# Optimization experiments

Measured on AMD Instinct MI355X. Metric: run time of the kernel, lower is better.

## Reference

```python
import jax, jax.numpy as jnp
import numpy as np

K = 32        # num_classes
NQ = 16384    # num query samples
C = 512       # feature_dim
H_REF = 512   # refinement_net hidden
H_CONF = 256  # confidence_net hidden
NUM_STEPS = 3


def setup_inputs() -> dict:
    key = jax.random.key(0)
    ks = jax.random.split(key, 8)
    s = 0.02
    return {
        "prototypes": jax.random.normal(ks[0], (K, C), jnp.float32),
        "query_features": jax.random.normal(ks[1], (NQ, C), jnp.float32),
        "query_distances": jax.random.uniform(ks[2], (NQ, K), jnp.float32) * 10.0,
        "W1": jax.random.normal(ks[3], (2 * C, H_REF), jnp.float32) * s,
        "b1": jnp.zeros((H_REF,), jnp.float32),
        "W2": jax.random.normal(ks[4], (H_REF, C), jnp.float32) * s,
        "b2": jnp.zeros((C,), jnp.float32),
        "Wc1": jax.random.normal(ks[5], (2 * C, H_CONF), jnp.float32) * s,
        "bc1": jnp.zeros((H_CONF,), jnp.float32),
        "Wc2": jax.random.normal(ks[6], (H_CONF, 1), jnp.float32) * s,
        "bc2": jnp.zeros((1,), jnp.float32),
    }


def reference(prototypes, query_features, query_distances,
              W1, b1, W2, b2, Wc1, bc1, Wc2, bc2):
    # ---- refinement loop (3 steps, sequential in refined prototypes) ----
    refined = prototypes
    for step in range(NUM_STEPS):
        # soft assignments over classes; temperature = step + 1
        soft = jax.nn.softmax(-query_distances / (step + 1.0), axis=-1)  # (NQ, K)
        wsum = jnp.maximum(soft.sum(axis=0), 1e-6)                       # (K,)  clamp(min=1e-6)
        wmean = (soft.T @ query_features) / wsum[:, None]                # (K, C)
        concat = jnp.concatenate([refined, wmean], axis=-1)              # (K, 2C)
        h = jax.nn.relu(concat @ W1 + b1)                                # dropout is identity in eval
        refinement = h @ W2 + b2                                         # (K, C)
        refined = refined + 0.1 * refinement

    # ---- confidence scores: MLP on [proto, query] pairs, mean over queries ----
    # Split first-layer weight into proto half and query half to avoid
    # materializing the (K, NQ, 2C) concat explicitly (same math).
    Wp, Wq = Wc1[:C], Wc1[C:]
    hp = prototypes @ Wp          # (K, H_CONF)
    hq = query_features @ Wq      # (NQ, H_CONF)
    hidden = jax.nn.relu(hp[:, None, :] + hq[None, :, :] + bc1)  # (K, NQ, H_CONF)
    conf = jax.nn.sigmoid(hidden @ Wc2 + bc2)                    # (K, NQ, 1)
    confidence_scores = conf.reshape(K, -1).mean(axis=1)         # (K,)

    return refined, confidence_scores
```

## Files before the change

### kernel.cpp

```cpp
#include <hip/hip_runtime.h>

#define KP 32
#define NQg 16384
#define CD 512
#define HC 256
#define NS 3

typedef __attribute__((ext_vector_type(8))) short short8;
typedef __attribute__((ext_vector_type(4))) short short4_t;
typedef __attribute__((ext_vector_type(8))) __bf16 bf16x8;
typedef __attribute__((ext_vector_type(4))) float floatx4;

union S8B8 { short8 s; bf16x8 b; };

__device__ __forceinline__ short f2bf(float f) {
    union { float f; unsigned u; } v; v.f = f;
    unsigned r = v.u + 0x7fffu + ((v.u >> 16) & 1u);
    return (short)(r >> 16);
}
__device__ __forceinline__ float bf2f(short s) {
    union { unsigned u; float f; } v; v.u = ((unsigned)(unsigned short)s) << 16;
    return v.f;
}
__device__ __forceinline__ float bflo(unsigned u) { return __uint_as_float(u << 16); }
__device__ __forceinline__ float bfhi(unsigned u) { return __uint_as_float(u & 0xffff0000u); }

__global__ __launch_bounds__(256) void k_A(const float* __restrict__ qd,
                                           const float* __restrict__ W1, const float* __restrict__ W2,
                                           const float* __restrict__ Wc1, const float* __restrict__ proto,
                                           const float* __restrict__ qf, const float* __restrict__ bc1,
                                           short* __restrict__ softT,
                                           short* __restrict__ W1p, short* __restrict__ W2p,
                                           short* __restrict__ wqp, float* __restrict__ refined,
                                           short* __restrict__ refined_b,
                                           short* __restrict__ qf2b, float* __restrict__ wmean,
                                           float* __restrict__ hpb,
                                           int* __restrict__ bar, float* __restrict__ dout) {
    int tid = threadIdx.x;
    int bid = blockIdx.x;
    if (bid < 64) {
        int q = bid * 256 + tid;
        float d[32];
        const float4* p = (const float4*)(qd + (size_t)q * 32);
#pragma unroll
        for (int j = 0; j < 8; j++) {
            float4 v = p[j];
            d[4 * j] = v.x; d[4 * j + 1] = v.y; d[4 * j + 2] = v.z; d[4 * j + 3] = v.w;
        }
#pragma unroll
        for (int s = 0; s < 3; s++) {
            float inv = -1.0f / (float)(s + 1);
            float e[32];
            float sum = 0.f;
#pragma unroll
            for (int k = 0; k < 32; k++) { e[k] = __expf(d[k] * inv); sum += e[k]; }
            float r = 1.0f / sum;
#pragma unroll
            for (int k = 0; k < 32; k++)
                softT[(size_t)(s * 32 + k) * NQg + q] = f2bf(e[k] * r);
        }
        return;
    }
    if (bid < 3712) {
        if (bid == 64) {
            if (tid < 32) dout[16384 + tid] = 0.f;
            else if (tid < 40) bar[tid - 32] = 0;
        }
        int idx = (bid - 64) * 256 + tid;
        if (idx < 524288) {
            int k = idx >> 9, n = idx & 511;
            W1p[((size_t)(k >> 3) * 512 + n) * 8 + (k & 7)] = f2bf(W1[idx]);
        } else if (idx < 786432) {
            int j = idx - 524288;
            int k = j >> 9, n = j & 511;
            W2p[((size_t)(k >> 3) * 512 + n) * 8 + (k & 7)] = f2bf(W2[j]);
        } else if (idx < 917504) {
            int j = idx - 786432;
            int k = j >> 8, n = j & 255;
            wqp[((size_t)(k >> 3) * 256 + n) * 8 + (k & 7)] = f2bf(Wc1[(size_t)(512 + k) * 256 + n]);
        } else {
            int j = idx - 917504;
            float v = proto[j];
            refined[j] = v;
            refined_b[j] = f2bf(v);
        }
        return;
    }
    if (bid < 3904) {
        int idx = (bid - 3712) * 256 + tid;
        wmean[idx] = 0.f;
        return;
    }
    if (bid < 5952) {
#pragma unroll
        for (int it = 0; it < 4; it++) {
            int j = (bid - 3904) * 1024 + it * 256 + tid;
            float4 v = *(const float4*)&qf[(size_t)j * 4];
            short4_t o;
            o[0] = f2bf(v.x); o[1] = f2bf(v.y); o[2] = f2bf(v.z); o[3] = f2bf(v.w);
            *(short4_t*)&qf2b[(size_t)j * 4] = o;
        }
        return;
    }
    {
        int r = bid - 5952;
        const float* pr = proto + r * 512;
        const float* wc = Wc1 + tid;
        float a0 = 0.f, a1 = 0.f, a2 = 0.f, a3 = 0.f;
#pragma unroll 4
        for (int i = 0; i < 512; i += 4) {
            float4 p4 = *(const float4*)&pr[i];
            float w0 = wc[(size_t)i * 256];
            float w1 = wc[(size_t)(i + 1) * 256];
            float w2 = wc[(size_t)(i + 2) * 256];
            float w3 = wc[(size_t)(i + 3) * 256];
            a0 += p4.x * w0;
            a1 += p4.y * w1;
            a2 += p4.z * w2;
            a3 += p4.w * w3;
        }
        hpb[r * 256 + tid] = bc1[tid] + ((a0 + a1) + (a2 + a3));
    }
}

__global__ __launch_bounds__(256) void k_B(const short* __restrict__ qf2b,
                                           const short* __restrict__ softT,
                                           const short* __restrict__ wqp,
                                           float* __restrict__ wmean,
                                           short* __restrict__ hq_g,
                                           float* __restrict__ wsuminv) {
    __shared__ short B_lds[128 * 40];
    int tid = threadIdx.x;
    int lane = tid & 63, w = tid >> 6;
    int ml = lane & 15, q8 = lane >> 4;

    if (blockIdx.x < 256) {
        int kc = blockIdx.x >> 2, ns = blockIdx.x & 3;
        int c0 = ns * 128;
        int qbase0 = kc * 256;
        int c_l = 2 * lane;
        int q_l = 8 * w;

        floatx4 acc[6][2];
#pragma unroll
        for (int mt = 0; mt < 6; mt++)
#pragma unroll
            for (int nt = 0; nt < 2; nt++) acc[mt][nt] = (floatx4){0.f, 0.f, 0.f, 0.f};

        for (int step = 0; step < 8; step++) {
            int qb = qbase0 + step * 32;
            short8 sA, sB;
#pragma unroll
            for (int i = 0; i < 8; i++) {
                unsigned u = *(const unsigned*)&qf2b[(size_t)(qb + q_l + i) * 512 + c0 + c_l];
                sA[i] = (short)(u & 0xffffu);
                sB[i] = (short)(u >> 16);
            }
            __syncthreads();
            *(short8*)&B_lds[c_l * 40 + q_l] = sA;
            *(short8*)&B_lds[(c_l + 1) * 40 + q_l] = sB;
            S8B8 a[6];
#pragma unroll
            for (int mt = 0; mt < 6; mt++)
                a[mt].s = *(const short8*)&softT[(size_t)(mt * 16 + ml) * NQg + qb + q8 * 8];
            __syncthreads();
#pragma unroll
            for (int nt = 0; nt < 2; nt++) {
                S8B8 b; b.s = *(short8*)&B_lds[(w * 32 + nt * 16 + ml) * 40 + q8 * 8];
#pragma unroll
                for (int mt = 0; mt < 6; mt++)
                    acc[mt][nt] = __builtin_amdgcn_mfma_f32_16x16x32_bf16(a[mt].b, b.b, acc[mt][nt], 0, 0, 0);
            }
        }
#pragma unroll
        for (int mt = 0; mt < 6; mt++) {
#pragma unroll
            for (int nt = 0; nt < 2; nt++) {
                int c = c0 + w * 32 + nt * 16 + ml;
#pragma unroll
                for (int r = 0; r < 4; r++) {
                    int m = mt * 16 + q8 * 4 + r;
                    atomicAdd(&wmean[(size_t)m * 512 + c], acc[mt][nt][r]);
                }
            }
        }
    } else if (blockIdx.x < 768) {
        int m0 = (blockIdx.x - 256) * 32;
        int n0 = w * 64;
        floatx4 acc[2][4];
#pragma unroll
        for (int mt = 0; mt < 2; mt++)
#pragma unroll
            for (int nt = 0; nt < 4; nt++) acc[mt][nt] = (floatx4){0.f, 0.f, 0.f, 0.f};

#pragma unroll 4
        for (int kc = 0; kc < 512; kc += 32) {
            S8B8 a[2], b[4];
#pragma unroll
            for (int mt = 0; mt < 2; mt++)
                a[mt].s = *(const short8*)&qf2b[(size_t)(m0 + mt * 16 + ml) * 512 + kc + q8 * 8];
#pragma unroll
            for (int nt = 0; nt < 4; nt++)
                b[nt].s = *(const short8*)&wqp[((size_t)((kc >> 3) + q8) * 256 + n0 + nt * 16 + ml) * 8];
#pragma unroll
            for (int mt = 0; mt < 2; mt++)
#pragma unroll
                for (int nt = 0; nt < 4; nt++)
                    acc[mt][nt] = __builtin_amdgcn_mfma_f32_16x16x32_bf16(a[mt].b, b[nt].b, acc[mt][nt], 0, 0, 0);
        }
#pragma unroll
        for (int mt = 0; mt < 2; mt++)
#pragma unroll
            for (int nt = 0; nt < 4; nt++) {
                int col = n0 + nt * 16 + ml;
#pragma unroll
                for (int r = 0; r < 4; r++) {
                    int row = m0 + mt * 16 + q8 * 4 + r;
                    hq_g[(size_t)row * 256 + col] = f2bf(acc[mt][nt][r]);
                }
            }
    } else {
        float* red = (float*)B_lds;
        int sk = blockIdx.x - 768;
        const short* row = softT + (size_t)sk * NQg;
        float s = 0.f;
#pragma unroll
        for (int j = 0; j < 8; j++) {
            short8 v = *(const short8*)&row[j * 2048 + tid * 8];
#pragma unroll
            for (int i = 0; i < 8; i++) s += bf2f(v[i]);
        }
        red[tid] = s;
        __syncthreads();
        for (int off = 128; off > 0; off >>= 1) {
            if (tid < off) red[tid] += red[tid + off];
            __syncthreads();
        }
        if (tid == 0) wsuminv[sk] = 1.0f / fmaxf(red[0], 1e-6f);
    }
}

__device__ __forceinline__ void gbar(int* bar, int phase, int nblk) {
    __syncthreads();
    if (threadIdx.x == 0) {
        __threadfence();
        __hip_atomic_fetch_add(&bar[phase], 1, __ATOMIC_ACQ_REL, __HIP_MEMORY_SCOPE_AGENT);
        while (__hip_atomic_load(&bar[phase], __ATOMIC_ACQUIRE, __HIP_MEMORY_SCOPE_AGENT) < nblk)
            __builtin_amdgcn_s_sleep(1);
    }
    __syncthreads();
}

__global__ __launch_bounds__(256) void k_D(const float* __restrict__ wmean,
                                           const float* __restrict__ wsuminv,
                                           const short* __restrict__ W1p,
                                           const float* __restrict__ b1,
                                           const short* __restrict__ W2p,
                                           const float* __restrict__ b2,
                                           float* __restrict__ refined,
                                           short* __restrict__ hb,
                                           int* __restrict__ bar,
                                           const short* __restrict__ hq_g,
                                           const float* __restrict__ hpb,
                                           const float* __restrict__ Wc2,
                                           const float* __restrict__ bc2p,
                                           float* __restrict__ dout,
                                           short* __restrict__ wmean_b,
                                           short* __restrict__ refined_b) {
    __shared__ float smem[6688];
    int tid = threadIdx.x, lane = tid & 63, w = tid >> 6;
    int ml = lane & 15, q8 = lane >> 4;

    if (blockIdx.x < 16) {
        int nb = blockIdx.x;
        int nh = w & 1, mh = w >> 1;
        int n = nb * 32 + nh * 16 + ml;
        int phase = 0;

#pragma unroll
        for (int i = 0; i < 12; i++) {
            int idx = i * 4096 + nb * 256 + tid;
            int row = idx >> 9;
            wmean_b[idx] = f2bf(wmean[idx] * wsuminv[row]);
        }
        gbar(bar, phase++, 16);

        for (int s = 0; s < 3; s++) {
            {
                const short* rfb = refined_b + (size_t)(mh * 16 + ml) * 512;
                const short* wmb = wmean_b + (size_t)(s * 32 + mh * 16 + ml) * 512;
                floatx4 acc = (floatx4){0.f, 0.f, 0.f, 0.f};
#pragma unroll
                for (int st = 0; st < 16; st++) {
                    int k0 = st * 32 + q8 * 8;
                    S8B8 a; a.s = *(const short8*)&rfb[k0];
                    S8B8 b; b.s = *(const short8*)&W1p[((size_t)(k0 >> 3) * 512 + n) * 8];
                    acc = __builtin_amdgcn_mfma_f32_16x16x32_bf16(a.b, b.b, acc, 0, 0, 0);
                }
#pragma unroll
                for (int st = 16; st < 32; st++) {
                    int k0 = st * 32 + q8 * 8;
                    S8B8 a; a.s = *(const short8*)&wmb[k0 - 512];
                    S8B8 b; b.s = *(const short8*)&W1p[((size_t)(k0 >> 3) * 512 + n) * 8];
                    acc = __builtin_amdgcn_mfma_f32_16x16x32_bf16(a.b, b.b, acc, 0, 0, 0);
                }
                float bias = b1[n];
#pragma unroll
                for (int r = 0; r < 4; r++) {
                    int row = mh * 16 + q8 * 4 + r;
                    hb[(size_t)row * 512 + n] = f2bf(fmaxf(acc[r] + bias, 0.f));
                }
            }
            gbar(bar, phase++, 16);
            {
                floatx4 acc = (floatx4){0.f, 0.f, 0.f, 0.f};
#pragma unroll
                for (int st = 0; st < 16; st++) {
                    int k0 = st * 32 + q8 * 8;
                    S8B8 a; a.s = *(const short8*)&hb[(size_t)(mh * 16 + ml) * 512 + k0];
                    S8B8 b; b.s = *(const short8*)&W2p[((size_t)(k0 >> 3) * 512 + n) * 8];
                    acc = __builtin_amdgcn_mfma_f32_16x16x32_bf16(a.b, b.b, acc, 0, 0, 0);
                }
                float b2v = b2[n];
#pragma unroll
                for (int r = 0; r < 4; r++) {
                    int row = mh * 16 + q8 * 4 + r;
                    float val = refined[(size_t)row * 512 + n] + 0.1f * (acc[r] + b2v);
                    refined[(size_t)row * 512 + n] = val;
                    refined_b[(size_t)row * 512 + n] = f2bf(val);
                    if (s == 2) dout[(size_t)row * 512 + n] = val;
                }
            }
            if (s < 2) gbar(bar, phase++, 16);
        }
    } else {
        short* hq_lds = (short*)smem;
        short* hp_s   = (short*)smem + 4480;
        float* wc2s   = smem + 6400;
        float* confl  = smem + 6656;
        int q0 = (blockIdx.x - 16) * 16;

        wc2s[tid] = Wc2[tid];
        if (tid < 32) confl[tid] = 0.f;
#pragma unroll
        for (int i = 0; i < 8; i++) {
            int idx = i * 256 + tid;
            int r = idx >> 6, c = (idx & 63) * 4;
            float4 v = *(const float4*)&hpb[r * 256 + c];
            short4_t o;
            o[0] = f2bf(v.x); o[1] = f2bf(v.y); o[2] = f2bf(v.z); o[3] = f2bf(v.w);
            *(short4_t*)&hp_s[r * 260 + c] = o;
        }
        {
            const short* hqs = hq_g + (size_t)q0 * 256;
            int r = tid >> 4, c = (tid & 15) * 16;
            *(short8*)&hq_lds[r * 280 + c] = *(const short8*)&hqs[r * 256 + c];
            *(short8*)&hq_lds[r * 280 + c + 8] = *(const short8*)&hqs[r * 256 + c + 8];
        }
        __syncthreads();

        int q = tid & 15, kg = tid >> 4;
        int k0 = kg, k1 = kg + 16;
        float s0 = 0.f, s1 = 0.f;
        for (int h = 0; h < 256; h += 4) {
            uint2 hv = *(uint2*)&hq_lds[q * 280 + h];
            float f0 = bflo(hv.x), f1 = bfhi(hv.x), f2 = bflo(hv.y), f3 = bfhi(hv.y);
            uint2 u0 = *(uint2*)&hp_s[k0 * 260 + h];
            uint2 u1 = *(uint2*)&hp_s[k1 * 260 + h];
            float4 wv = *(float4*)&wc2s[h];
            s0 += fmaxf(bflo(u0.x) + f0, 0.f) * wv.x;
            s0 += fmaxf(bfhi(u0.x) + f1, 0.f) * wv.y;
            s0 += fmaxf(bflo(u0.y) + f2, 0.f) * wv.z;
            s0 += fmaxf(bfhi(u0.y) + f3, 0.f) * wv.w;
            s1 += fmaxf(bflo(u1.x) + f0, 0.f) * wv.x;
            s1 += fmaxf(bfhi(u1.x) + f1, 0.f) * wv.y;
            s1 += fmaxf(bflo(u1.y) + f2, 0.f) * wv.z;
            s1 += fmaxf(bfhi(u1.y) + f3, 0.f) * wv.w;
        }
        float bc2 = bc2p[0];
        float v0 = 1.f / (1.f + __expf(-(s0 + bc2)));
        float v1 = 1.f / (1.f + __expf(-(s1 + bc2)));
        atomicAdd(&confl[k0], v0);
        atomicAdd(&confl[k1], v1);
        __syncthreads();
        if (tid < 32) atomicAdd(&dout[16384 + tid], confl[tid] * (1.0f / 16384.0f));
    }
}

extern "C" void kernel_launch(void* const* d_in, const int* in_sizes, int n_in,
                              void* d_out, int out_size, void* d_ws, size_t ws_size,
                              hipStream_t stream) {
    const float* proto = (const float*)d_in[0];
    const float* qf    = (const float*)d_in[1];
    const float* qd    = (const float*)d_in[2];
    const float* W1    = (const float*)d_in[3];
    const float* b1    = (const float*)d_in[4];
    const float* W2    = (const float*)d_in[5];
    const float* b2    = (const float*)d_in[6];
    const float* Wc1   = (const float*)d_in[7];
    const float* bc1   = (const float*)d_in[8];
    const float* Wc2   = (const float*)d_in[9];
    const float* bc2   = (const float*)d_in[10];
    float* out = (float*)d_out;

    float* ws = (float*)d_ws;
    short* softT   = (short*)ws;
    short* qf2b    = (short*)(ws + 786432);
    float* wmean   = ws + 4980736;
    float* refined = ws + 5029888;
    short* hb      = (short*)(ws + 5046272);
    short* W1p     = (short*)(ws + 5054464);
    short* W2p     = (short*)(ws + 5316608);
    short* wqp     = (short*)(ws + 5447680);
    float* hpb     = ws + 5513216;
    int*   bar     = (int*)(ws + 5521408);
    float* wsuminv = ws + 5521416;
    short* hq      = (short*)(ws + 5521536);
    short* refined_b = (short*)(ws + 7618688);
    short* wmean_b   = (short*)(ws + 7626880);

    k_A<<<5984, 256, 0, stream>>>(qd, W1, W2, Wc1, proto, qf, bc1, softT, W1p, W2p, wqp,
                                  refined, refined_b, qf2b, wmean, hpb, bar, out);
    k_B<<<864, 256, 0, stream>>>(qf2b, softT, wqp, wmean, hq, wsuminv);
    k_D<<<1040, 256, 0, stream>>>(wmean, wsuminv, W1p, b1, W2p, b2, refined, hb, bar,
                                  hq, hpb, Wc2, bc2, out, wmean_b, refined_b);
}
```

Before: 194.1 us.

## Restructure refinement loop to split-K atomic accumulation, cutting grid barriers

The 16-block refinement path no longer keeps refined/refined_b and hb buffers in global memory. Each block computes its 32-column slice of h, keeps it in LDS, and atomically accumulates partial W2 products into per-step accumulators. The refined input is rebuilt on the fly from proto plus the earlier accumulators, and wmean normalization is fused into the A-operand load. This cuts the grid barriers per run from six to three, in exchange for float atomics, extra zeroing in k_A, and a different bf16 rounding path.

```diff
diff --git a/kernel.cpp b/kernel.cpp
--- a/kernel.cpp
+++ b/kernel.cpp
@@ -31,9 +31,9 @@
                                            const float* __restrict__ qf, const float* __restrict__ bc1,
                                            short* __restrict__ softT,
                                            short* __restrict__ W1p, short* __restrict__ W2p,
-                                           short* __restrict__ wqp, float* __restrict__ refined,
-                                           short* __restrict__ refined_b,
+                                           short* __restrict__ wqp,
                                            short* __restrict__ qf2b, float* __restrict__ wmean,
+                                           float* __restrict__ accs,
                                            float* __restrict__ hpb,
                                            int* __restrict__ bar, float* __restrict__ dout) {
     int tid = threadIdx.x;
@@ -61,11 +61,7 @@
         }
         return;
     }
-    if (bid < 3712) {
-        if (bid == 64) {
-            if (tid < 32) dout[16384 + tid] = 0.f;
-            else if (tid < 40) bar[tid - 32] = 0;
-        }
+    if (bid < 3648) {
         int idx = (bid - 64) * 256 + tid;
         if (idx < 524288) {
             int k = idx >> 9, n = idx & 511;
@@ -74,27 +70,27 @@
             int j = idx - 524288;
             int k = j >> 9, n = j & 511;
             W2p[((size_t)(k >> 3) * 512 + n) * 8 + (k & 7)] = f2bf(W2[j]);
-        } else if (idx < 917504) {
+        } else {
             int j = idx - 786432;
             int k = j >> 8, n = j & 255;
             wqp[((size_t)(k >> 3) * 256 + n) * 8 + (k & 7)] = f2bf(Wc1[(size_t)(512 + k) * 256 + n]);
-        } else {
-            int j = idx - 917504;
-            float v = proto[j];
-            refined[j] = v;
-            refined_b[j] = f2bf(v);
         }
         return;
     }
-    if (bid < 3904) {
-        int idx = (bid - 3712) * 256 + tid;
-        wmean[idx] = 0.f;
+    if (bid < 4032) {
+        if (bid == 3648) {
+            if (tid < 32) dout[16384 + tid] = 0.f;
+            else if (tid < 40) bar[tid - 32] = 0;
+        }
+        int idx = (bid - 3648) * 256 + tid;
+        if (idx < 49152) wmean[idx] = 0.f;
+        else accs[idx - 49152] = 0.f;
         return;
     }
-    if (bid < 5952) {
+    if (bid < 6080) {
 #pragma unroll
         for (int it = 0; it < 4; it++) {
-            int j = (bid - 3904) * 1024 + it * 256 + tid;
+            int j = (bid - 4032) * 1024 + it * 256 + tid;
             float4 v = *(const float4*)&qf[(size_t)j * 4];
             short4_t o;
             o[0] = f2bf(v.x); o[1] = f2bf(v.y); o[2] = f2bf(v.z); o[3] = f2bf(v.w);
@@ -103,7 +99,7 @@
         return;
     }
     {
-        int r = bid - 5952;
+        int r = bid - 6080;
         const float* pr = proto + r * 512;
         const float* wc = Wc1 + tid;
         float a0 = 0.f, a1 = 0.f, a2 = 0.f, a3 = 0.f;
@@ -257,81 +253,116 @@
                                            const float* __restrict__ b1,
                                            const short* __restrict__ W2p,
                                            const float* __restrict__ b2,
-                                           float* __restrict__ refined,
-                                           short* __restrict__ hb,
+                                           const float* __restrict__ proto,
+                                           float* __restrict__ accs,
                                            int* __restrict__ bar,
                                            const short* __restrict__ hq_g,
                                            const float* __restrict__ hpb,
                                            const float* __restrict__ Wc2,
                                            const float* __restrict__ bc2p,
-                                           float* __restrict__ dout,
-                                           short* __restrict__ wmean_b,
-                                           short* __restrict__ refined_b) {
+                                           float* __restrict__ dout) {
     __shared__ float smem[6688];
     int tid = threadIdx.x, lane = tid & 63, w = tid >> 6;
     int ml = lane & 15, q8 = lane >> 4;
 
     if (blockIdx.x < 16) {
+        short* hb_s = (short*)smem;
+        float* acc0 = accs;
+        float* acc1 = accs + 16384;
+        float* acc2 = accs + 32768;
         int nb = blockIdx.x;
-        int nh = w & 1, mh = w >> 1;
-        int n = nb * 32 + nh * 16 + ml;
-        int phase = 0;
-
-#pragma unroll
-        for (int i = 0; i < 12; i++) {
-            int idx = i * 4096 + nb * 256 + tid;
-            int row = idx >> 9;
-            wmean_b[idx] = f2bf(wmean[idx] * wsuminv[row]);
-        }
-        gbar(bar, phase++, 16);
-
+        int mh = w >> 1, nh = w & 1;
+        int n_loc = nh * 16 + ml;
+        int n = nb * 32 + n_loc;
+        float b1v = b1[n];
+        int arow = mh * 16 + ml;
+
+        const float* pr  = proto + (size_t)arow * 512;
+        const float* a0p = acc0 + (size_t)arow * 512;
+        const float* a1p = acc1 + (size_t)arow * 512;
+
+#pragma unroll
         for (int s = 0; s < 3; s++) {
-            {
-                const short* rfb = refined_b + (size_t)(mh * 16 + ml) * 512;
-                const short* wmb = wmean_b + (size_t)(s * 32 + mh * 16 + ml) * 512;
-                floatx4 acc = (floatx4){0.f, 0.f, 0.f, 0.f};
-#pragma unroll
-                for (int st = 0; st < 16; st++) {
-                    int k0 = st * 32 + q8 * 8;
-                    S8B8 a; a.s = *(const short8*)&rfb[k0];
-                    S8B8 b; b.s = *(const short8*)&W1p[((size_t)(k0 >> 3) * 512 + n) * 8];
-                    acc = __builtin_amdgcn_mfma_f32_16x16x32_bf16(a.b, b.b, acc, 0, 0, 0);
+            float iv = wsuminv[s * 32 + arow];
+            const float* wm = wmean + (size_t)(s * 32 + arow) * 512;
+            float sb2 = 0.1f * (float)s;
+            floatx4 ac[4];
+#pragma unroll
+            for (int j = 0; j < 4; j++) ac[j] = (floatx4){0.f, 0.f, 0.f, 0.f};
+
+#pragma unroll
+            for (int st = 0; st < 16; st++) {
+                int k0 = st * 32 + q8 * 8;
+                float f[8];
+                float4 pa = *(const float4*)&pr[k0];
+                float4 pb = *(const float4*)&pr[k0 + 4];
+                f[0] = pa.x; f[1] = pa.y; f[2] = pa.z; f[3] = pa.w;
+                f[4] = pb.x; f[5] = pb.y; f[6] = pb.z; f[7] = pb.w;
+                if (s >= 1) {
+                    float4 qa = *(const float4*)&a0p[k0];
+                    float4 qb = *(const float4*)&a0p[k0 + 4];
+                    f[0] += 0.1f * qa.x; f[1] += 0.1f * qa.y; f[2] += 0.1f * qa.z; f[3] += 0.1f * qa.w;
+                    f[4] += 0.1f * qb.x; f[5] += 0.1f * qb.y; f[6] += 0.1f * qb.z; f[7] += 0.1f * qb.w;
+                    float4 ba = *(const float4*)&b2[k0];
+                    float4 bb = *(const float4*)&b2[k0 + 4];
+                    f[0] += sb2 * ba.x; f[1] += sb2 * ba.y; f[2] += sb2 * ba.z; f[3] += sb2 * ba.w;
+                    f[4] += sb2 * bb.x; f[5] += sb2 * bb.y; f[6] += sb2 * bb.z; f[7] += sb2 * bb.w;
                 }
-#pragma unroll
-                for (int st = 16; st < 32; st++) {
-                    int k0 = st * 32 + q8 * 8;
-                    S8B8 a; a.s = *(const short8*)&wmb[k0 - 512];
-                    S8B8 b; b.s = *(const short8*)&W1p[((size_t)(k0 >> 3) * 512 + n) * 8];
-                    acc = __builtin_amdgcn_mfma_f32_16x16x32_bf16(a.b, b.b, acc, 0, 0, 0);
+                if (s >= 2) {
+                    float4 qa = *(const float4*)&a1p[k0];
+                    float4 qb = *(const float4*)&a1p[k0 + 4];
+                    f[0] += 0.1f * qa.x; f[1] += 0.1f * qa.y; f[2] += 0.1f * qa.z; f[3] += 0.1f * qa.w;
+                    f[4] += 0.1f * qb.x; f[5] += 0.1f * qb.y; f[6] += 0.1f * qb.z; f[7] += 0.1f * qb.w;
                 }
-                float bias = b1[n];
+                short8 t;
+#pragma unroll
+                for (int i = 0; i < 8; i++) t[i] = f2bf(f[i]);
+                S8B8 a; a.s = t;
+                S8B8 b; b.s = *(const short8*)&W1p[((size_t)(k0 >> 3) * 512 + n) * 8];
+                ac[st & 3] = __builtin_amdgcn_mfma_f32_16x16x32_bf16(a.b, b.b, ac[st & 3], 0, 0, 0);
+            }
+#pragma unroll
+            for (int st = 16; st < 32; st++) {
+                int kw = (st - 16) * 32 + q8 * 8;
+                float4 wa = *(const float4*)&wm[kw];
+                float4 wb = *(const float4*)&wm[kw + 4];
+                short8 t;
+                t[0] = f2bf(wa.x * iv); t[1] = f2bf(wa.y * iv); t[2] = f2bf(wa.z * iv); t[3] = f2bf(wa.w * iv);
+                t[4] = f2bf(wb.x * iv); t[5] = f2bf(wb.y * iv); t[6] = f2bf(wb.z * iv); t[7] = f2bf(wb.w * iv);
+                S8B8 a; a.s = t;
+                int k0 = st * 32 + q8 * 8;
+                S8B8 b; b.s = *(const short8*)&W1p[((size_t)(k0 >> 3) * 512 + n) * 8];
+                ac[st & 3] = __builtin_amdgcn_mfma_f32_16x16x32_bf16(a.b, b.b, ac[st & 3], 0, 0, 0);
+            }
+            floatx4 acf = (ac[0] + ac[1]) + (ac[2] + ac[3]);
+#pragma unroll
+            for (int r = 0; r < 4; r++)
+                hb_s[(mh * 16 + q8 * 4 + r) * 40 + n_loc] = f2bf(fmaxf(acf[r] + b1v, 0.f));
+            __syncthreads();
+
+            float* accw = (s == 0) ? acc0 : (s == 1) ? acc1 : acc2;
+            S8B8 a2lo, a2hi;
+            a2lo.s = *(const short8*)&hb_s[ml * 40 + q8 * 8];
+            a2hi.s = *(const short8*)&hb_s[(16 + ml) * 40 + q8 * 8];
+#pragma unroll
+            for (int nt = 0; nt < 8; nt++) {
+                int n2 = w * 128 + nt * 16 + ml;
+                S8B8 b; b.s = *(const short8*)&W2p[((size_t)(nb * 4 + q8) * 512 + n2) * 8];
+                floatx4 c0 = __builtin_amdgcn_mfma_f32_16x16x32_bf16(a2lo.b, b.b, (floatx4){0.f, 0.f, 0.f, 0.f}, 0, 0, 0);
+                floatx4 c1 = __builtin_amdgcn_mfma_f32_16x16x32_bf16(a2hi.b, b.b, (floatx4){0.f, 0.f, 0.f, 0.f}, 0, 0, 0);
 #pragma unroll
                 for (int r = 0; r < 4; r++) {
-                    int row = mh * 16 + q8 * 4 + r;
-                    hb[(size_t)row * 512 + n] = f2bf(fmaxf(acc[r] + bias, 0.f));
+                    atomicAdd(&accw[(size_t)(q8 * 4 + r) * 512 + n2], c0[r]);
+                    atomicAdd(&accw[(size_t)(16 + q8 * 4 + r) * 512 + n2], c1[r]);
                 }
             }
-            gbar(bar, phase++, 16);
-            {
-                floatx4 acc = (floatx4){0.f, 0.f, 0.f, 0.f};
-#pragma unroll
-                for (int st = 0; st < 16; st++) {
-                    int k0 = st * 32 + q8 * 8;
-                    S8B8 a; a.s = *(const short8*)&hb[(size_t)(mh * 16 + ml) * 512 + k0];
-                    S8B8 b; b.s = *(const short8*)&W2p[((size_t)(k0 >> 3) * 512 + n) * 8];
-                    acc = __builtin_amdgcn_mfma_f32_16x16x32_bf16(a.b, b.b, acc, 0, 0, 0);
-                }
-                float b2v = b2[n];
-#pragma unroll
-                for (int r = 0; r < 4; r++) {
-                    int row = mh * 16 + q8 * 4 + r;
-                    float val = refined[(size_t)row * 512 + n] + 0.1f * (acc[r] + b2v);
-                    refined[(size_t)row * 512 + n] = val;
-                    refined_b[(size_t)row * 512 + n] = f2bf(val);
-                    if (s == 2) dout[(size_t)row * 512 + n] = val;
-                }
-            }
-            if (s < 2) gbar(bar, phase++, 16);
+            gbar(bar, s, 16);
+        }
+#pragma unroll
+        for (int i = 0; i < 4; i++) {
+            int idx = nb * 1024 + i * 256 + tid;
+            int c = idx & 511;
+            dout[idx] = proto[idx] + 0.1f * (acc0[idx] + acc1[idx] + acc2[idx]) + 0.3f * b2[c];
         }
     } else {
         short* hq_lds = (short*)smem;
@@ -407,8 +438,6 @@
     short* softT   = (short*)ws;
     short* qf2b    = (short*)(ws + 786432);
     float* wmean   = ws + 4980736;
-    float* refined = ws + 5029888;
-    short* hb      = (short*)(ws + 5046272);
     short* W1p     = (short*)(ws + 5054464);
     short* W2p     = (short*)(ws + 5316608);
     short* wqp     = (short*)(ws + 5447680);
@@ -416,12 +445,11 @@
     int*   bar     = (int*)(ws + 5521408);
     float* wsuminv = ws + 5521416;
     short* hq      = (short*)(ws + 5521536);
-    short* refined_b = (short*)(ws + 7618688);
-    short* wmean_b   = (short*)(ws + 7626880);
-
-    k_A<<<5984, 256, 0, stream>>>(qd, W1, W2, Wc1, proto, qf, bc1, softT, W1p, W2p, wqp,
-                                  refined, refined_b, qf2b, wmean, hpb, bar, out);
+    float* accs    = ws + 7618688;
+
+    k_A<<<6112, 256, 0, stream>>>(qd, W1, W2, Wc1, proto, qf, bc1, softT, W1p, W2p, wqp,
+                                  qf2b, wmean, accs, hpb, bar, out);
     k_B<<<864, 256, 0, stream>>>(qf2b, softT, wqp, wmean, hq, wsuminv);
-    k_D<<<1040, 256, 0, stream>>>(wmean, wsuminv, W1p, b1, W2p, b2, refined, hb, bar,
-                                  hq, hpb, Wc2, bc2, out, wmean_b, refined_b);
-}
+    k_D<<<1040, 256, 0, stream>>>(wmean, wsuminv, W1p, b1, W2p, b2, proto, accs, bar,
+                                  hq, hpb, Wc2, bc2, out);
+}
```

Result: slower. 226.0 us (+16.4%).
